# Performance work log

Measured on AMD Instinct MI355X. Metric: run time of the kernel, lower is better.

The kernel has to match this reference:

```python
import jax, jax.numpy as jnp
import numpy as np

# irreps_node_input = 64x0e + 16x1e  -> 64 scalars + 16 vectors (dim 112)
N_S = 64      # scalar channels
N_V = 16      # vector channels
H = 8         # attention heads
RBF = 128     # radial basis size
MID = 64      # radial MLP hidden
NW = N_S * 2 + N_V * 3   # 176 TP path weights per edge
ALPHA_C = (N_S + N_V) // H   # 80 scalars -> 10 per head
VEC_C = (N_S + N_V + N_V) // H  # 96 vec channels -> 12 per head


def _smooth_leaky(x, a=0.2):
    # SmoothLeakyReLU: x * (a + (1-a)*sigmoid(x))
    return x * (a + (1.0 - a) * jax.nn.sigmoid(x))


def _ln(x, eps=1e-5):
    m = jnp.mean(x, axis=-1, keepdims=True)
    v = jnp.var(x, axis=-1, keepdims=True)
    return (x - m) * jax.lax.rsqrt(v + eps)


def setup_inputs() -> dict:
    N, E = 50000, 400000
    key = jax.random.key(0)
    ks = jax.random.split(key, 16)
    D = N_S + 3 * N_V
    inp = {}
    inp['node_input'] = jax.random.normal(ks[0], (N, D), dtype=jnp.float32)
    inp['edge_src'] = jax.random.randint(ks[1], (E,), 0, N)
    inp['edge_dst'] = jax.random.randint(ks[2], (E,), 0, N)
    inp['edge_attr'] = jax.random.normal(ks[3], (E, 4), dtype=jnp.float32)      # sh: 1x0e+1x1e
    inp['edge_scalars'] = jax.random.normal(ks[4], (E, RBF), dtype=jnp.float32)  # RBF features
    # per-irrep linear weights (LinearRS style, 1/sqrt(fan_in) scale)
    inp['w_src_s'] = jax.random.normal(ks[5], (N_S, N_S), dtype=jnp.float32) / np.sqrt(N_S)
    inp['w_src_v'] = jax.random.normal(ks[6], (N_V, N_V), dtype=jnp.float32) / np.sqrt(N_V)
    inp['w_dst_s'] = jax.random.normal(ks[7], (N_S, N_S), dtype=jnp.float32) / np.sqrt(N_S)
    inp['w_dst_v'] = jax.random.normal(ks[8], (N_V, N_V), dtype=jnp.float32) / np.sqrt(N_V)
    # RadialProfile MLP
    inp['rad_w1'] = jax.random.normal(ks[9], (RBF, MID), dtype=jnp.float32) / np.sqrt(RBF)
    inp['rad_b1'] = jnp.zeros((MID,), dtype=jnp.float32)
    inp['rad_w2'] = jax.random.normal(ks[10], (MID, NW), dtype=jnp.float32) / np.sqrt(MID)
    inp['rad_b2'] = jnp.zeros((NW,), dtype=jnp.float32)
    # per-head alpha dot vector
    inp['alpha_dot'] = jax.random.normal(ks[11], (H, ALPHA_C), dtype=jnp.float32) / np.sqrt(ALPHA_C)
    # output projection (per-irrep)
    inp['proj_ws'] = jax.random.normal(ks[12], (N_S + N_V, N_S), dtype=jnp.float32) / np.sqrt(N_S + N_V)
    inp['proj_bs'] = jnp.zeros((N_S,), dtype=jnp.float32)
    inp['proj_wv'] = jax.random.normal(ks[13], (N_S + 2 * N_V, N_V), dtype=jnp.float32) / np.sqrt(N_S + 2 * N_V)
    return inp


def reference(node_input, edge_attr, edge_scalars, w_src_s, w_src_v, w_dst_s, w_dst_v,
              rad_w1, rad_b1, rad_w2, rad_b2, alpha_dot, proj_ws, proj_bs, proj_wv,
              edge_src, edge_dst):
    N = node_input.shape[0]
    E = edge_src.shape[0]
    s_in = node_input[:, :N_S]                              # [N, 64]
    v_in = node_input[:, N_S:].reshape(N, N_V, 3)           # [N, 16, 3]
    # merge_src / merge_dst equivariant linears, then gather onto edges
    s = (s_in @ w_src_s)[edge_src] + (s_in @ w_dst_s)[edge_dst]                    # [E, 64]
    v = jnp.einsum('ncd,ce->ned', v_in, w_src_v)[edge_src] \
        + jnp.einsum('ncd,ce->ned', v_in, w_dst_v)[edge_dst]                       # [E, 16, 3]
    e0 = edge_attr[:, 0]                                     # [E] 0e sh
    e1 = edge_attr[:, 1:4]                                   # [E, 3] 1e sh
    # RadialProfile: per-edge TP weights
    h = jax.nn.silu(_ln(edge_scalars @ rad_w1 + rad_b1))
    w = h @ rad_w2 + rad_b2                                  # [E, 176]
    w0 = w[:, :N_S]                  # 0e x 0e -> 0e
    w1 = w[:, N_S:2 * N_S]           # 0e x 1e -> 1e
    w2 = w[:, 2 * N_S:2 * N_S + N_V]             # 1e x 0e -> 1e
    w3 = w[:, 2 * N_S + N_V:2 * N_S + 2 * N_V]   # 1e x 1e -> 0e
    w4 = w[:, 2 * N_S + 2 * N_V:]                # 1e x 1e -> 1e
    inv_s3 = 1.0 / np.sqrt(3.0)
    inv_s2 = 1.0 / np.sqrt(2.0)
    # depthwise (uvu) tensor product, outputs sorted even-first: [64x0e, 16x0e, 64x1e, 16x1e, 16x1e]
    out_s = jnp.concatenate([
        w0 * s * e0[:, None],
        w3 * jnp.einsum('ekd,ed->ek', v, e1) * inv_s3,
    ], axis=1)                                               # [E, 80]
    out_v = jnp.concatenate([
        (w1 * s)[:, :, None] * e1[:, None, :],
        w2[:, :, None] * v * e0[:, None, None],
        w4[:, :, None] * jnp.cross(v, e1[:, None, :]) * inv_s2,
    ], axis=1)                                               # [E, 96, 3]
    # heads
    a_feat = out_s.reshape(E, H, ALPHA_C)                    # [E, 8, 10]
    alpha = jnp.einsum('ehc,hc->eh', _smooth_leaky(a_feat), alpha_dot)  # [E, 8]
    # segment softmax over destination nodes
    amax = jax.ops.segment_max(alpha, edge_dst, num_segments=N)
    amax = jnp.where(jnp.isfinite(amax), amax, 0.0)
    ex = jnp.exp(alpha - amax[edge_dst])
    den = jax.ops.segment_sum(ex, edge_dst, num_segments=N)
    attn = ex / (den[edge_dst] + 1e-9)                       # [E, 8]
    # values per head: scalars + flattened vector channels
    value = jnp.concatenate([a_feat, out_v.reshape(E, H, VEC_C * 3)], axis=2)  # [E, 8, 46]
    agg = jax.ops.segment_sum(attn[:, :, None] * value, edge_dst, num_segments=N)  # [N, 8, 46]
    s_agg = agg[:, :, :ALPHA_C].reshape(N, H * ALPHA_C)      # [N, 80]
    v_agg = agg[:, :, ALPHA_C:].reshape(N, H * VEC_C, 3)     # [N, 96, 3]
    # output projection (per-irrep linear with bias on scalars)
    out_sf = s_agg @ proj_ws + proj_bs                       # [N, 64]
    out_vf = jnp.einsum('ncd,ce->ned', v_agg, proj_wv).reshape(N, N_V * 3)  # [N, 48]
    return jnp.concatenate([out_sf, out_vf], axis=1)         # [N, 112]
```

## Files before the change

kernel.cpp:

```cpp
#include <hip/hip_runtime.h>
#include <hip/hip_bf16.h>

#define WST 184
#define CROW 264

typedef __attribute__((ext_vector_type(8))) short bf16x8;
typedef __attribute__((ext_vector_type(4))) float f32x4;

__device__ inline ushort f2bf(float f){
  union { __hip_bfloat16 b; ushort u; } v;
  v.b = __float2bfloat16(f);
  return v.u;
}
__device__ inline ushort f2h(float f){ _Float16 h=(_Float16)f; ushort u; __builtin_memcpy(&u,&h,2); return u; }
__device__ inline float h2f(ushort u){ _Float16 h; __builtin_memcpy(&h,&u,2); return (float)h; }

__global__ __launch_bounds__(256) void k_node(
  const float* __restrict__ ni,
  const float* __restrict__ wss, const float* __restrict__ wsv,
  const float* __restrict__ wds, const float* __restrict__ wdv,
  float* __restrict__ xs_s, float* __restrict__ xs_d,
  float* __restrict__ xv_s, float* __restrict__ xv_d, int N)
{
  __shared__ float sW0[64*64], sW1[64*64];
  __shared__ float sV0[256], sV1[256];
  __shared__ float sRow[4][112];
  int t = threadIdx.x, wid = t>>6, lane = t&63;
  for(int i=t;i<4096;i+=256){ sW0[i]=wss[i]; sW1[i]=wds[i]; }
  if(t<256){ sV0[t]=wsv[t]; sV1[t]=wdv[t]; }
  __syncthreads();
  for(int itn=0; itn<16; ++itn){
    int node = blockIdx.x*64 + itn*4 + wid;
    if(node>=N) continue;
    const float* row = ni + (size_t)node*112;
    if(lane<56) ((float2*)sRow[wid])[lane] = ((const float2*)row)[lane];
    float* r = sRow[wid];
    float a0=0.f, a1=0.f;
    #pragma unroll 8
    for(int k=0;k<64;k++){ float x=r[k]; a0+=x*sW0[k*64+lane]; a1+=x*sW1[k*64+lane]; }
    xs_s[(size_t)node*64+lane]=a0; xs_d[(size_t)node*64+lane]=a1;
    if(lane<48){
      int e_=lane/3, d_=lane-e_*3; float b0=0.f, b1=0.f;
      #pragma unroll
      for(int c=0;c<16;c++){ float x=r[64+c*3+d_]; b0+=x*sV0[c*16+e_]; b1+=x*sV1[c*16+e_]; }
      xv_s[(size_t)node*48+lane]=b0; xv_d[(size_t)node*48+lane]=b1;
    }
  }
}

__global__ void k_deg(const int* __restrict__ edst, int* __restrict__ deg, int E){
  int e = blockIdx.x*256 + threadIdx.x;
  if(e<E) atomicAdd(&deg[edst[e]], 1);
}

__global__ __launch_bounds__(256) void k_scan1(
  const int* __restrict__ deg, int* __restrict__ cur, int* __restrict__ bsum, int N)
{
  __shared__ int sb[256];
  int t = threadIdx.x, i = blockIdx.x*256 + t;
  int x = (i<N) ? deg[i] : 0;
  sb[t]=x; __syncthreads();
  int v=x;
  #pragma unroll
  for(int o=1;o<256;o<<=1){
    int u=(t>=o)?sb[t-o]:0; __syncthreads();
    v+=u; sb[t]=v; __syncthreads();
  }
  if(i<N) cur[i]=v-x;
  if(t==255) bsum[blockIdx.x]=v;
}

__global__ __launch_bounds__(256) void k_scan2(
  int* __restrict__ bsum, int* __restrict__ offs, int N, int nb)
{
  __shared__ int sb[256];
  int t = threadIdx.x;
  int x = (t<nb) ? bsum[t] : 0;
  sb[t]=x; __syncthreads();
  int v=x;
  #pragma unroll
  for(int o=1;o<256;o<<=1){
    int u=(t>=o)?sb[t-o]:0; __syncthreads();
    v+=u; sb[t]=v; __syncthreads();
  }
  if(t<nb) bsum[t]=v-x;
  if(t==nb-1) offs[N]=v;
}

__global__ void k_scan3(const int* __restrict__ bsum,
                        int* __restrict__ offs, int* __restrict__ cur, int N)
{
  int i = blockIdx.x*256 + threadIdx.x;
  if(i<N){ int v = cur[i] + bsum[blockIdx.x]; offs[i]=v; cur[i]=v; }
}

__global__ void k_fill(const int* __restrict__ edst, int* __restrict__ cur,
                       int* __restrict__ pos_of, int E){
  int e = blockIdx.x*256 + threadIdx.x;
  if(e<E) pos_of[e] = atomicAdd(&cur[edst[e]], 1);
}

__global__ __launch_bounds__(256) void k_mlp(
  const float* __restrict__ escal,
  const float* __restrict__ w1, const float* __restrict__ b1,
  const float* __restrict__ w2, const float* __restrict__ b2,
  _Float16* __restrict__ wbuf, int E)
{
  __shared__ __align__(16) ushort sW1t[64*136];
  __shared__ __align__(16) ushort sW2t[176*72];
  __shared__ __align__(16) ushort ubuf[4][16*WST];
  int t = threadIdx.x, wid = t>>6, lane = t&63;
  int r16 = lane&15, g = lane>>4;

  for(int i=t;i<128*64;i+=256){ int k=i>>6, n=i&63; sW1t[n*136+k]=f2bf(w1[i]); }
  for(int i=t;i<64*176;i+=256){ int k=i/176, n=i-k*176; sW2t[n*72+k]=f2bf(w2[i]); }
  __syncthreads();

  float b1v[4], b2v[11];
  #pragma unroll
  for(int nt=0;nt<4;nt++) b1v[nt]=b1[nt*16+r16];
  #pragma unroll
  for(int s=0;s<11;s++) b2v[s]=b2[s*16+r16];

  ushort* ub = ubuf[wid];
  _Float16* wsb = (_Float16*)ub;

  int ntiles = (E+15)>>4;
  int nw = gridDim.x*4;

  for(int wt = blockIdx.x*4+wid; wt < ntiles; wt += nw){
    int ebase = wt*16;
    int erow = ebase + r16; if(erow >= E) erow = E-1;

    f32x4 acc[4];
    #pragma unroll
    for(int nt=0;nt<4;nt++) acc[nt]=(f32x4){0,0,0,0};
    #pragma unroll
    for(int ks=0;ks<4;ks++){
      const float* p = escal + (size_t)erow*128 + ks*32 + g*8;
      float4 va = *(const float4*)p;
      float4 vb = *(const float4*)(p+4);
      bf16x8 af;
      af[0]=(short)f2bf(va.x); af[1]=(short)f2bf(va.y);
      af[2]=(short)f2bf(va.z); af[3]=(short)f2bf(va.w);
      af[4]=(short)f2bf(vb.x); af[5]=(short)f2bf(vb.y);
      af[6]=(short)f2bf(vb.z); af[7]=(short)f2bf(vb.w);
      #pragma unroll
      for(int nt=0;nt<4;nt++){
        bf16x8 bf = *(const bf16x8*)&sW1t[(nt*16+r16)*136 + ks*32 + g*8];
        acc[nt] = __builtin_amdgcn_mfma_f32_16x16x32_bf16(af,bf,acc[nt],0,0,0);
      }
    }

    #pragma unroll
    for(int nt=0;nt<4;nt++)
      #pragma unroll
      for(int q=0;q<4;q++) acc[nt][q] += b1v[nt];
    #pragma unroll
    for(int q=0;q<4;q++){
      float s = acc[0][q]+acc[1][q]+acc[2][q]+acc[3][q];
      float ss = acc[0][q]*acc[0][q]+acc[1][q]*acc[1][q]+acc[2][q]*acc[2][q]+acc[3][q]*acc[3][q];
      #pragma unroll
      for(int o=1;o<16;o<<=1){ s += __shfl_xor(s,o); ss += __shfl_xor(ss,o); }
      float m = s*(1.f/64.f);
      float var = ss*(1.f/64.f) - m*m;
      float inv = rsqrtf(var + 1e-5f);
      int rr = g*4+q;
      #pragma unroll
      for(int nt=0;nt<4;nt++){
        float xn = (acc[nt][q]-m)*inv;
        float h = xn/(1.f+__expf(-xn));
        ub[rr*72 + nt*16 + r16] = f2bf(h);
      }
    }

    bf16x8 af2[2];
    af2[0] = *(const bf16x8*)&ub[r16*72 + 0*32 + g*8];
    af2[1] = *(const bf16x8*)&ub[r16*72 + 1*32 + g*8];
    f32x4 c2[11];
    #pragma unroll
    for(int s=0;s<11;s++) c2[s]=(f32x4){0,0,0,0};
    #pragma unroll
    for(int ks=0;ks<2;ks++){
      #pragma unroll
      for(int s=0;s<11;s++){
        bf16x8 bf = *(const bf16x8*)&sW2t[(s*16+r16)*72 + ks*32 + g*8];
        c2[s] = __builtin_amdgcn_mfma_f32_16x16x32_bf16(af2[ks],bf,c2[s],0,0,0);
      }
    }
    #pragma unroll
    for(int s=0;s<11;s++){
      int col = s*16 + r16;
      #pragma unroll
      for(int q=0;q<4;q++){
        wsb[(g*4+q)*WST + col] = (_Float16)(c2[s][q] + b2v[s]);
      }
    }
    int rows = E - ebase; if(rows > 16) rows = 16;
    int nf4 = rows*(WST/8);
    float4* dst = (float4*)(wbuf + (size_t)ebase*WST);
    const float4* srcv = (const float4*)ub;
    for(int i=lane; i<nf4; i+=64) dst[i] = srcv[i];
  }
}

__global__ __launch_bounds__(256) void k_geo(
  const int* __restrict__ esrc, const int* __restrict__ edst,
  const float* __restrict__ eattr, const _Float16* __restrict__ wbuf,
  const float* __restrict__ adot,
  const float* __restrict__ xs_s, const float* __restrict__ xs_d,
  const float* __restrict__ xv_s, const float* __restrict__ xv_d,
  const int* __restrict__ pos_of,
  _Float16* __restrict__ cbuf, float* __restrict__ alphaC, int E)
{
  __shared__ float sAdot[80];
  __shared__ float sV[4][48];
  __shared__ float sP[4][80];
  int t = threadIdx.x, wid = t>>6, lane = t&63;
  if(t<80) sAdot[t]=adot[t];
  __syncthreads();

  float* V = sV[wid];
  float* P = sP[wid];
  int nw = gridDim.x*4;
  const float inv_s3 = 0.5773502691896258f, inv_s2 = 0.7071067811865475f;

  int l3 = lane/3;
  int d  = lane - l3*3;
  int k3 = l3*3;
  int d1 = (d==2)?0:d+1;
  int d2 = (d==0)?2:d-1;

  for(int e = blockIdx.x*4+wid; e < E; e += nw){
    int p = pos_of[e], si = esrc[e], di = edst[e];
    float4 ea = *(const float4*)&eattr[(size_t)e*4];
    const _Float16* wr = wbuf + (size_t)e*WST;
    float S = xs_s[(size_t)si*64+lane] + xs_d[(size_t)di*64+lane];
    float Vl = 0.f;
    if(lane<48){ Vl = xv_s[(size_t)si*48+lane] + xv_d[(size_t)di*48+lane]; V[lane]=Vl; }
    float w0 = (float)wr[lane];
    float w1v = (float)wr[64+lane];
    float sc = w0*S*ea.x;
    float sg = 1.f/(1.f+__expf(-sc));
    P[lane] = sc*(0.2f + 0.8f*sg)*sAdot[lane];
    float sc2 = 0.f;
    if(lane<16){
      float vd3 = V[lane*3]*ea.y + V[lane*3+1]*ea.z + V[lane*3+2]*ea.w;
      sc2 = (float)wr[144+lane]*vd3*inv_s3;
      float sg2 = 1.f/(1.f+__expf(-sc2));
      P[64+lane] = sc2*(0.2f + 0.8f*sg2)*sAdot[64+lane];
    }
    if(lane<8){
      float a = P[lane*10];
      #pragma unroll
      for(int c=1;c<10;c++) a += P[lane*10+c];
      alphaC[(size_t)p*8+lane] = a;
    }
    float scBv = __shfl(sc2, lane&15);
    float wslot = scBv;
    if(lane<48){
      float e1d1 = (d1==0)?ea.y:((d1==1)?ea.z:ea.w);
      float e1d2 = (d2==0)?ea.y:((d2==1)?ea.z:ea.w);
      float cr = V[k3+d1]*e1d2 - V[k3+d2]*e1d1;
      wslot = (float)wr[160+l3]*cr*inv_s2;
    }
    float w2v_pre = (lane<48) ? (float)wr[128+l3]*ea.x*Vl : 0.f;
    ushort4 ck;
    ck.x = f2h(w1v*S);
    ck.y = f2h(w2v_pre);
    ck.z = f2h(sc);
    ck.w = f2h(wslot);
    _Float16* cr_ = cbuf + (size_t)p*CROW;
    *(ushort4*)(cr_ + (size_t)lane*4) = ck;
    if(lane==0) *(float4*)((char*)cr_ + 512) = ea;
  }
}

#define EDGE_PROC(b, ck_, ea_, w1x,w1y,w1z,sc,aa,xx,den) { \
  float ev_ = 0.f; \
  if(lane<8){ ev_ = __expf(alphaC[(size_t)(b)*8+lane] - mx); den += ev_; } \
  float evW1_ = __shfl(ev_,hW1), evSC_ = __shfl(ev_,hSC); \
  float evA_ = __shfl(ev_,hA), evX_ = __shfl(ev_,hX); \
  float ws1_ = h2f(ck_.x), scA_ = h2f(ck_.z), wv_ = h2f(ck_.w); \
  float vA_ = (lane<48) ? h2f(ck_.y) : wv_; \
  float t1_ = evW1_*ws1_; \
  w1x += t1_*ea_.y; w1y += t1_*ea_.z; w1z += t1_*ea_.w; \
  sc += evSC_*scA_; aa += evA_*vA_; xx += evX_*wv_; }

__global__ __launch_bounds__(256) void k_agg(
  const int* __restrict__ offs, const float* __restrict__ alphaC,
  const _Float16* __restrict__ cbuf,
  const float* __restrict__ pws, const float* __restrict__ pbs,
  const float* __restrict__ pwv, float* __restrict__ out, int N)
{
  __shared__ float sVa[4][288];
  __shared__ float sSa[4][80];
  int t=threadIdx.x, wid=t>>6, lane=t&63;

  float* Va = sVa[wid];
  float* Sa = sSa[wid];

  int l3 = lane/3;
  int d  = lane - l3*3;
  int hW1 = lane/12;
  int hX  = (80+l3)/12;
  int hSC = lane/10;
  int hA  = (lane<48) ? (64+l3)/12 : (64+(lane-48))/10;
  int h8 = lane&7;

  int nw4 = gridDim.x*4;
  for(int n = blockIdx.x*4+wid; n < N; n += nw4){
    int s0 = offs[n], s1 = offs[n+1];

    float mx = -1e30f;
    for(int b = s0 + (lane>>3); b < s1; b += 8)
      mx = fmaxf(mx, alphaC[(size_t)b*8 + h8]);
    mx = fmaxf(mx, __shfl_xor(mx, 8));
    mx = fmaxf(mx, __shfl_xor(mx, 16));
    mx = fmaxf(mx, __shfl_xor(mx, 32));

    float denA=0.f, w1xA=0.f,w1yA=0.f,w1zA=0.f,scA=0.f,aaA=0.f,xxA=0.f;
    float denB=0.f, w1xB=0.f,w1yB=0.f,w1zB=0.f,scB=0.f,aaB=0.f,xxB=0.f;
    int b = s0;
    for(; b+3 < s1; b += 4){
      const _Float16* c0 = cbuf + (size_t)(b  )*CROW;
      const _Float16* c1 = cbuf + (size_t)(b+1)*CROW;
      const _Float16* c2 = cbuf + (size_t)(b+2)*CROW;
      const _Float16* c3 = cbuf + (size_t)(b+3)*CROW;
      ushort4 k0 = *(const ushort4*)(c0 + (size_t)lane*4);
      ushort4 k1 = *(const ushort4*)(c1 + (size_t)lane*4);
      ushort4 k2 = *(const ushort4*)(c2 + (size_t)lane*4);
      ushort4 k3v= *(const ushort4*)(c3 + (size_t)lane*4);
      float4 e0 = *(const float4*)((const char*)c0 + 512);
      float4 e1 = *(const float4*)((const char*)c1 + 512);
      float4 e2 = *(const float4*)((const char*)c2 + 512);
      float4 e3 = *(const float4*)((const char*)c3 + 512);
      EDGE_PROC(b,   k0, e0, w1xA,w1yA,w1zA,scA,aaA,xxA,denA)
      EDGE_PROC(b+1, k1, e1, w1xB,w1yB,w1zB,scB,aaB,xxB,denB)
      EDGE_PROC(b+2, k2, e2, w1xA,w1yA,w1zA,scA,aaA,xxA,denA)
      EDGE_PROC(b+3, k3v,e3, w1xB,w1yB,w1zB,scB,aaB,xxB,denB)
    }
    for(; b < s1; ++b){
      const _Float16* c0 = cbuf + (size_t)b*CROW;
      ushort4 k0 = *(const ushort4*)(c0 + (size_t)lane*4);
      float4 e0 = *(const float4*)((const char*)c0 + 512);
      EDGE_PROC(b, k0, e0, w1xA,w1yA,w1zA,scA,aaA,xxA,denA)
    }
    float den = denA+denB;
    float w1x=w1xA+w1xB, w1y=w1yA+w1yB, w1z=w1zA+w1zB;
    float sc=scA+scB, aa=aaA+aaB, xx=xxA+xxB;

    float dnW1 = __shfl(den, hW1) + 1e-9f;
    float dnSC = __shfl(den, hSC) + 1e-9f;
    float dnA  = __shfl(den, hA)  + 1e-9f;
    float dnX  = __shfl(den, hX)  + 1e-9f;

    Va[lane*3+0] = w1x/dnW1;
    Va[lane*3+1] = w1y/dnW1;
    Va[lane*3+2] = w1z/dnW1;
    if(lane<48){
      Va[192+lane] = aa/dnA;
      Va[240+lane] = xx/dnX;
    } else {
      Sa[64+(lane-48)] = aa/dnA;
    }
    Sa[lane] = sc/dnSC;

    float o1 = pbs[lane];
    #pragma unroll 8
    for(int i=0;i<80;i++) o1 += Sa[i]*pws[i*64+lane];
    out[(size_t)n*112+lane] = o1;
    if(lane<48){
      float o2 = 0.f;
      #pragma unroll 8
      for(int k=0;k<64;k++) o2 += Va[k*3+d]*pwv[k*16+l3];
      #pragma unroll
      for(int k=0;k<16;k++) o2 += Va[192+k*3+d]*pwv[(64+k)*16+l3];
      #pragma unroll
      for(int k=0;k<16;k++) o2 += Va[240+k*3+d]*pwv[(80+k)*16+l3];
      out[(size_t)n*112+64+lane] = o2;
    }
  }
}

extern "C" void kernel_launch(void* const* d_in, const int* in_sizes, int n_in,
                              void* d_out, int out_size, void* d_ws, size_t ws_size,
                              hipStream_t stream)
{
  const int N = in_sizes[0]/112;
  const int E = in_sizes[1];
  const float* ni    = (const float*)d_in[0];
  const int*   esrc  = (const int*)d_in[1];
  const int*   edst  = (const int*)d_in[2];
  const float* eattr = (const float*)d_in[3];
  const float* escal = (const float*)d_in[4];
  const float* wss   = (const float*)d_in[5];
  const float* wsv   = (const float*)d_in[6];
  const float* wds   = (const float*)d_in[7];
  const float* wdv   = (const float*)d_in[8];
  const float* rw1   = (const float*)d_in[9];
  const float* rb1   = (const float*)d_in[10];
  const float* rw2   = (const float*)d_in[11];
  const float* rb2   = (const float*)d_in[12];
  const float* adot  = (const float*)d_in[13];
  const float* pws   = (const float*)d_in[14];
  const float* pbs   = (const float*)d_in[15];
  const float* pwv   = (const float*)d_in[16];
  float* out = (float*)d_out;

  char* ws = (char*)d_ws;
  size_t off = 0;
  auto alloc = [&](size_t bytes)->void*{
    void* p = ws + off;
    off = (off + bytes + 255) & ~(size_t)255;
    return p;
  };
  float*    xs_s  = (float*)   alloc((size_t)N*64*4);
  float*    xs_d  = (float*)   alloc((size_t)N*64*4);
  float*    xv_s  = (float*)   alloc((size_t)N*48*4);
  float*    xv_d  = (float*)   alloc((size_t)N*48*4);
  _Float16* wbuf  = (_Float16*)alloc((size_t)E*WST*2);
  _Float16* cbuf  = (_Float16*)alloc((size_t)E*CROW*2);
  float*    alphaC= (float*)   alloc((size_t)E*8*4);
  int*      pos_of= (int*)     alloc((size_t)E*4);
  int*      deg   = (int*)     alloc((size_t)N*4);
  int*      offs  = (int*)     alloc((size_t)(N+1)*4);
  int*      cur   = (int*)     alloc((size_t)N*4);
  int*      bsum  = (int*)     alloc(256*4);

  const int nb = (N+255)/256;

  hipMemsetAsync(deg, 0, (size_t)N*4, stream);

  k_node<<<(N+63)/64, 256, 0, stream>>>(ni, wss, wsv, wds, wdv, xs_s, xs_d, xv_s, xv_d, N);
  k_deg<<<(E+255)/256, 256, 0, stream>>>(edst, deg, E);
  k_scan1<<<nb, 256, 0, stream>>>(deg, cur, bsum, N);
  k_scan2<<<1, 256, 0, stream>>>(bsum, offs, N, nb);
  k_scan3<<<nb, 256, 0, stream>>>(bsum, offs, cur, N);
  k_fill<<<(E+255)/256, 256, 0, stream>>>(edst, cur, pos_of, E);

  k_mlp<<<512, 256, 0, stream>>>(escal, rw1, rb1, rw2, rb2, wbuf, E);

  k_geo<<<2048, 256, 0, stream>>>(esrc, edst, eattr, wbuf, adot,
        xs_s, xs_d, xv_s, xv_d, pos_of, cbuf, alphaC, E);

  k_agg<<<2048, 256, 0, stream>>>(offs, alphaC, cbuf, pws, pbs, pwv, out, N);
}
```

Measured before the change: 677.3 us.

## Iterate k_geo in dst-sorted order; scatter MLP weights; shuffle-based softmax

k_fill now writes dst-sorted copies of src, dst and edge attributes, and k_mlp scatters its per-edge weight rows to the sorted position. k_geo can then iterate directly over sorted positions, so consecutive waves read adjacent dst nodes and write cbuf/alphaC contiguously. k_geo also swaps LDS vector staging for wave shuffles and does a parallel head reduction. k_agg computes the per-lane head max and exp directly instead of shuffling exp/den values. The cost is extra scatter writes in k_mlp (non-contiguous rows) and more buffers and traffic in k_fill.

```diff
diff --git a/kernel.cpp b/kernel.cpp
--- a/kernel.cpp
+++ b/kernel.cpp
@@ -94,16 +94,25 @@
   if(i<N){ int v = cur[i] + bsum[blockIdx.x]; offs[i]=v; cur[i]=v; }
 }
 
-__global__ void k_fill(const int* __restrict__ edst, int* __restrict__ cur,
-                       int* __restrict__ pos_of, int E){
+__global__ void k_fill(const int* __restrict__ esrc, const int* __restrict__ edst,
+                       const float* __restrict__ eattr, int* __restrict__ cur,
+                       int* __restrict__ pos_of, int* __restrict__ srcC,
+                       int* __restrict__ dstC, float4* __restrict__ eaC, int E){
   int e = blockIdx.x*256 + threadIdx.x;
-  if(e<E) pos_of[e] = atomicAdd(&cur[edst[e]], 1);
+  if(e<E){
+    int p = atomicAdd(&cur[edst[e]], 1);
+    pos_of[e] = p;
+    srcC[p] = esrc[e];
+    dstC[p] = edst[e];
+    eaC[p] = *(const float4*)&eattr[(size_t)e*4];
+  }
 }
 
 __global__ __launch_bounds__(256) void k_mlp(
   const float* __restrict__ escal,
   const float* __restrict__ w1, const float* __restrict__ b1,
   const float* __restrict__ w2, const float* __restrict__ b2,
+  const int* __restrict__ pos_of,
   _Float16* __restrict__ wbuf, int E)
 {
   __shared__ __align__(16) ushort sW1t[64*136];
@@ -196,31 +205,33 @@
         wsb[(g*4+q)*WST + col] = (_Float16)(c2[s][q] + b2v[s]);
       }
     }
+    int pv = 0;
+    if(lane<16 && ebase+lane < E) pv = pos_of[ebase+lane];
     int rows = E - ebase; if(rows > 16) rows = 16;
-    int nf4 = rows*(WST/8);
-    float4* dst = (float4*)(wbuf + (size_t)ebase*WST);
     const float4* srcv = (const float4*)ub;
-    for(int i=lane; i<nf4; i+=64) dst[i] = srcv[i];
+    int tot4 = rows*23;
+    for(int i=lane; i<tot4; i+=64){
+      int r = i/23, c = i - 23*r;
+      int pos = __shfl(pv, r);
+      ((float4*)(wbuf + (size_t)pos*WST))[c] = srcv[i];
+    }
   }
 }
 
 __global__ __launch_bounds__(256) void k_geo(
-  const int* __restrict__ esrc, const int* __restrict__ edst,
-  const float* __restrict__ eattr, const _Float16* __restrict__ wbuf,
+  const int* __restrict__ srcC, const int* __restrict__ dstC,
+  const float4* __restrict__ eaC, const _Float16* __restrict__ wbuf,
   const float* __restrict__ adot,
   const float* __restrict__ xs_s, const float* __restrict__ xs_d,
   const float* __restrict__ xv_s, const float* __restrict__ xv_d,
-  const int* __restrict__ pos_of,
   _Float16* __restrict__ cbuf, float* __restrict__ alphaC, int E)
 {
   __shared__ float sAdot[80];
-  __shared__ float sV[4][48];
   __shared__ float sP[4][80];
   int t = threadIdx.x, wid = t>>6, lane = t&63;
   if(t<80) sAdot[t]=adot[t];
   __syncthreads();
 
-  float* V = sV[wid];
   float* P = sP[wid];
   int nw = gridDim.x*4;
   const float inv_s3 = 0.5773502691896258f, inv_s2 = 0.7071067811865475f;
@@ -230,41 +241,44 @@
   int k3 = l3*3;
   int d1 = (d==2)?0:d+1;
   int d2 = (d==0)?2:d-1;
-
-  for(int e = blockIdx.x*4+wid; e < E; e += nw){
-    int p = pos_of[e], si = esrc[e], di = edst[e];
-    float4 ea = *(const float4*)&eattr[(size_t)e*4];
-    const _Float16* wr = wbuf + (size_t)e*WST;
+  int l3c = l3&15;
+  int sA = (lane*3)&63, sB = (lane*3+1)&63, sC = (lane*3+2)&63;
+  int cs1 = (k3+d1)&63, cs2 = (k3+d2)&63;
+  int hh5 = (lane>>1)&7, st5 = hh5*10 + (lane&1)*5;
+  float adl = sAdot[lane];
+  float ad2 = sAdot[64+(lane&15)];
+
+  for(int p = blockIdx.x*4+wid; p < E; p += nw){
+    int si = srcC[p], di = dstC[p];
+    float4 ea = eaC[p];
+    const _Float16* wr = wbuf + (size_t)p*WST;
     float S = xs_s[(size_t)si*64+lane] + xs_d[(size_t)di*64+lane];
-    float Vl = 0.f;
-    if(lane<48){ Vl = xv_s[(size_t)si*48+lane] + xv_d[(size_t)di*48+lane]; V[lane]=Vl; }
+    float Vl = (lane<48) ? (xv_s[(size_t)si*48+lane] + xv_d[(size_t)di*48+lane]) : 0.f;
     float w0 = (float)wr[lane];
     float w1v = (float)wr[64+lane];
     float sc = w0*S*ea.x;
     float sg = 1.f/(1.f+__expf(-sc));
-    P[lane] = sc*(0.2f + 0.8f*sg)*sAdot[lane];
-    float sc2 = 0.f;
+    P[lane] = sc*(0.2f + 0.8f*sg)*adl;
+    float v0=__shfl(Vl,sA), v1=__shfl(Vl,sB), v2=__shfl(Vl,sC);
+    float vd3 = v0*ea.y + v1*ea.z + v2*ea.w;
+    float sc2 = (float)wr[144+(lane&15)]*vd3*inv_s3;
     if(lane<16){
-      float vd3 = V[lane*3]*ea.y + V[lane*3+1]*ea.z + V[lane*3+2]*ea.w;
-      sc2 = (float)wr[144+lane]*vd3*inv_s3;
       float sg2 = 1.f/(1.f+__expf(-sc2));
-      P[64+lane] = sc2*(0.2f + 0.8f*sg2)*sAdot[64+lane];
-    }
-    if(lane<8){
-      float a = P[lane*10];
-      #pragma unroll
-      for(int c=1;c<10;c++) a += P[lane*10+c];
-      alphaC[(size_t)p*8+lane] = a;
-    }
+      P[64+lane] = sc2*(0.2f + 0.8f*sg2)*ad2;
+    }
+    float s5 = P[st5] + P[st5+1] + P[st5+2] + P[st5+3] + P[st5+4];
+    float aL = __shfl(s5, 2*(lane&7)) + __shfl(s5, 2*(lane&7)+1);
+    if(lane<8) alphaC[(size_t)p*8+lane] = aL;
     float scBv = __shfl(sc2, lane&15);
+    float Vd1 = __shfl(Vl, cs1), Vd2 = __shfl(Vl, cs2);
     float wslot = scBv;
     if(lane<48){
       float e1d1 = (d1==0)?ea.y:((d1==1)?ea.z:ea.w);
       float e1d2 = (d2==0)?ea.y:((d2==1)?ea.z:ea.w);
-      float cr = V[k3+d1]*e1d2 - V[k3+d2]*e1d1;
-      wslot = (float)wr[160+l3]*cr*inv_s2;
-    }
-    float w2v_pre = (lane<48) ? (float)wr[128+l3]*ea.x*Vl : 0.f;
+      float cr = Vd1*e1d2 - Vd2*e1d1;
+      wslot = (float)wr[160+l3c]*cr*inv_s2;
+    }
+    float w2v_pre = (lane<48) ? (float)wr[128+l3c]*ea.x*Vl : 0.f;
     ushort4 ck;
     ck.x = f2h(w1v*S);
     ck.y = f2h(w2v_pre);
@@ -276,11 +290,13 @@
   }
 }
 
-#define EDGE_PROC(b, ck_, ea_, w1x,w1y,w1z,sc,aa,xx,den) { \
-  float ev_ = 0.f; \
-  if(lane<8){ ev_ = __expf(alphaC[(size_t)(b)*8+lane] - mx); den += ev_; } \
-  float evW1_ = __shfl(ev_,hW1), evSC_ = __shfl(ev_,hSC); \
-  float evA_ = __shfl(ev_,hA), evX_ = __shfl(ev_,hX); \
+#define EDGE_PROC(b, ck_, ea_, w1x,w1y,w1z,sc,aa,xx,dW1,dSC,dA,dX) { \
+  const float* ar_ = alphaC + (size_t)(b)*8; \
+  float evW1_ = __expf(ar_[hW1] - mxW1); \
+  float evSC_ = __expf(ar_[hSC] - mxSC); \
+  float evA_  = __expf(ar_[hA]  - mxA ); \
+  float evX_  = __expf(ar_[hX]  - mxX ); \
+  dW1 += evW1_; dSC += evSC_; dA += evA_; dX += evX_; \
   float ws1_ = h2f(ck_.x), scA_ = h2f(ck_.z), wv_ = h2f(ck_.w); \
   float vA_ = (lane<48) ? h2f(ck_.y) : wv_; \
   float t1_ = evW1_*ws1_; \
@@ -318,9 +334,13 @@
     mx = fmaxf(mx, __shfl_xor(mx, 8));
     mx = fmaxf(mx, __shfl_xor(mx, 16));
     mx = fmaxf(mx, __shfl_xor(mx, 32));
-
-    float denA=0.f, w1xA=0.f,w1yA=0.f,w1zA=0.f,scA=0.f,aaA=0.f,xxA=0.f;
-    float denB=0.f, w1xB=0.f,w1yB=0.f,w1zB=0.f,scB=0.f,aaB=0.f,xxB=0.f;
+    float mxW1 = __shfl(mx, hW1);
+    float mxSC = __shfl(mx, hSC);
+    float mxA  = __shfl(mx, hA);
+    float mxX  = __shfl(mx, hX);
+
+    float dW1A=0.f,dSCA=0.f,dAA=0.f,dXA=0.f, w1xA=0.f,w1yA=0.f,w1zA=0.f,scA=0.f,aaA=0.f,xxA=0.f;
+    float dW1B=0.f,dSCB=0.f,dAB=0.f,dXB=0.f, w1xB=0.f,w1yB=0.f,w1zB=0.f,scB=0.f,aaB=0.f,xxB=0.f;
     int b = s0;
     for(; b+3 < s1; b += 4){
       const _Float16* c0 = cbuf + (size_t)(b  )*CROW;
@@ -335,25 +355,23 @@
       float4 e1 = *(const float4*)((const char*)c1 + 512);
       float4 e2 = *(const float4*)((const char*)c2 + 512);
       float4 e3 = *(const float4*)((const char*)c3 + 512);
-      EDGE_PROC(b,   k0, e0, w1xA,w1yA,w1zA,scA,aaA,xxA,denA)
-      EDGE_PROC(b+1, k1, e1, w1xB,w1yB,w1zB,scB,aaB,xxB,denB)
-      EDGE_PROC(b+2, k2, e2, w1xA,w1yA,w1zA,scA,aaA,xxA,denA)
-      EDGE_PROC(b+3, k3v,e3, w1xB,w1yB,w1zB,scB,aaB,xxB,denB)
+      EDGE_PROC(b,   k0, e0, w1xA,w1yA,w1zA,scA,aaA,xxA,dW1A,dSCA,dAA,dXA)
+      EDGE_PROC(b+1, k1, e1, w1xB,w1yB,w1zB,scB,aaB,xxB,dW1B,dSCB,dAB,dXB)
+      EDGE_PROC(b+2, k2, e2, w1xA,w1yA,w1zA,scA,aaA,xxA,dW1A,dSCA,dAA,dXA)
+      EDGE_PROC(b+3, k3v,e3, w1xB,w1yB,w1zB,scB,aaB,xxB,dW1B,dSCB,dAB,dXB)
     }
     for(; b < s1; ++b){
       const _Float16* c0 = cbuf + (size_t)b*CROW;
       ushort4 k0 = *(const ushort4*)(c0 + (size_t)lane*4);
       float4 e0 = *(const float4*)((const char*)c0 + 512);
-      EDGE_PROC(b, k0, e0, w1xA,w1yA,w1zA,scA,aaA,xxA,denA)
-    }
-    float den = denA+denB;
+      EDGE_PROC(b, k0, e0, w1xA,w1yA,w1zA,scA,aaA,xxA,dW1A,dSCA,dAA,dXA)
+    }
+    float dnW1 = dW1A+dW1B + 1e-9f;
+    float dnSC = dSCA+dSCB + 1e-9f;
+    float dnA  = dAA +dAB  + 1e-9f;
+    float dnX  = dXA +dXB  + 1e-9f;
     float w1x=w1xA+w1xB, w1y=w1yA+w1yB, w1z=w1zA+w1zB;
     float sc=scA+scB, aa=aaA+aaB, xx=xxA+xxB;
-
-    float dnW1 = __shfl(den, hW1) + 1e-9f;
-    float dnSC = __shfl(den, hSC) + 1e-9f;
-    float dnA  = __shfl(den, hA)  + 1e-9f;
-    float dnX  = __shfl(den, hX)  + 1e-9f;
 
     Va[lane*3+0] = w1x/dnW1;
     Va[lane*3+1] = w1y/dnW1;
@@ -423,6 +441,9 @@
   _Float16* cbuf  = (_Float16*)alloc((size_t)E*CROW*2);
   float*    alphaC= (float*)   alloc((size_t)E*8*4);
   int*      pos_of= (int*)     alloc((size_t)E*4);
+  int*      srcC  = (int*)     alloc((size_t)E*4);
+  int*      dstC  = (int*)     alloc((size_t)E*4);
+  float4*   eaC   = (float4*)  alloc((size_t)E*16);
   int*      deg   = (int*)     alloc((size_t)N*4);
   int*      offs  = (int*)     alloc((size_t)(N+1)*4);
   int*      cur   = (int*)     alloc((size_t)N*4);
@@ -437,12 +458,12 @@
   k_scan1<<<nb, 256, 0, stream>>>(deg, cur, bsum, N);
   k_scan2<<<1, 256, 0, stream>>>(bsum, offs, N, nb);
   k_scan3<<<nb, 256, 0, stream>>>(bsum, offs, cur, N);
-  k_fill<<<(E+255)/256, 256, 0, stream>>>(edst, cur, pos_of, E);
-
-  k_mlp<<<512, 256, 0, stream>>>(escal, rw1, rb1, rw2, rb2, wbuf, E);
-
-  k_geo<<<2048, 256, 0, stream>>>(esrc, edst, eattr, wbuf, adot,
-        xs_s, xs_d, xv_s, xv_d, pos_of, cbuf, alphaC, E);
+  k_fill<<<(E+255)/256, 256, 0, stream>>>(esrc, edst, eattr, cur, pos_of, srcC, dstC, eaC, E);
+
+  k_mlp<<<512, 256, 0, stream>>>(escal, rw1, rb1, rw2, rb2, pos_of, wbuf, E);
+
+  k_geo<<<2048, 256, 0, stream>>>(srcC, dstC, eaC, wbuf, adot,
+        xs_s, xs_d, xv_s, xv_d, cbuf, alphaC, E);
 
   k_agg<<<2048, 256, 0, stream>>>(offs, alphaC, cbuf, pws, pbs, pwv, out, N);
 }
```

Result: faster. 644.2 us (-4.9%).
